# Performance work log

Measured on AMD Instinct MI355X. Metric: run time of the kernel, lower is better.

The kernel has to match this reference:

```python
import math
import jax, jax.numpy as jnp
import numpy as np

G_RATIO = 0.5
TB_FACTOR = 1e-3


def _expand(x):
    # x: [B,H,W]; 3x3 all-ones-except-center neighbor conv (same filter for every sample)
    k = jnp.ones((1, 1, 3, 3), x.dtype).at[0, 0, 1, 1].set(0.0)
    y = jax.lax.conv_general_dilated(x[:, None], k, (1, 1), 'SAME')
    return y[:, 0]


def _st_softmax_noexp(val):
    # straight-through normalized selection over flattened map
    B = val.shape[0]
    v = val.reshape(B, -1)
    y = v / v.sum(-1, keepdims=True)
    ind = jnp.argmax(y, -1)
    y_hard = jax.nn.one_hot(ind, y.shape[-1], dtype=y.dtype)
    y = y + jax.lax.stop_gradient(y_hard - y)
    return y.reshape(val.shape)


def _heuristic(gm):
    # gm: [B,H,W] one-hot goal maps -> Chebyshev + tb*Euclidean distance field
    B, H, W = gm.shape
    loc = jnp.stack(jnp.meshgrid(jnp.arange(H), jnp.arange(W), indexing='ij'), 0).astype(gm.dtype)  # [2,H,W]
    loc_e = loc.reshape(2, -1)[None]                      # [1,2,HW]
    goal_loc = jnp.einsum('kij,bij->bk', loc, gm)[:, :, None]  # [B,2,1]
    d = jnp.abs(loc_e - goal_loc)                         # [B,2,HW]
    h = d.sum(1) - d.min(1)
    euc = jnp.sqrt(((loc_e - goal_loc) ** 2).sum(1))
    return (h + TB_FACTOR * euc).reshape(B, H, W)


def _forward_core(cost_maps, start_maps, goal_maps, obstacles_maps):
    cm, sm, gm, om = cost_maps[:, 0], start_maps[:, 0], goal_maps[:, 0], obstacles_maps[:, 0]
    B, H, W = cm.shape
    h = _heuristic(gm) + cm
    goal_idx = jnp.argmax(gm.reshape(B, -1), -1)
    parents0 = jnp.broadcast_to(goal_idx[:, None].astype(cm.dtype), (B, H * W))
    inv_sqrt = 1.0 / math.sqrt(W)
    Tmax = W * W

    def step(carry, i):
        g, open_m, hist, parents, done, t = carry
        f = G_RATIO * g + (1.0 - G_RATIO) * h
        f_exp = jnp.exp(-f * inv_sqrt) * open_m
        snm = _st_softmax_noexp(f_exp)
        dist = (snm * gm).sum((1, 2), keepdims=True)
        unsolved = (dist < 1e-8).astype(cm.dtype)
        hist_n = jnp.clip(hist + snm, 0.0, 1.0)
        open_n = jnp.clip(open_m - unsolved * snm, 0.0, 1.0)
        nb = _expand(snm) * om
        g2 = _expand((g + cm) * snm)
        idx = ((1.0 - open_n) * (1.0 - hist_n) + open_n * (g > g2).astype(cm.dtype)) * nb
        idx = jax.lax.stop_gradient(idx)
        g_n = jax.lax.stop_gradient(g2 * idx + g * (1.0 - idx))
        open_n = jax.lax.stop_gradient(jnp.clip(open_n + idx, 0.0, 1.0))
        idx_f = idx.reshape(B, -1)
        new_par = jnp.argmax(snm.reshape(B, -1), -1)[:, None].astype(cm.dtype)
        par_n = new_par * idx_f + parents * (1.0 - idx_f)
        done_n = jnp.all(unsolved == 0)
        sel = lambda new, old: jnp.where(done, old, new)  # emulate the torch early break
        carry_n = (sel(g_n, g), sel(open_n, open_m), sel(hist_n, hist), sel(par_n, parents),
                   jnp.logical_or(done, done_n), jnp.where(done, t, i))
        return carry_n, None

    init = (jnp.zeros_like(sm), sm, jnp.zeros_like(sm), parents0,
            jnp.array(False), jnp.array(0, jnp.int32))
    (g, open_m, hist, parents, done, t), _ = jax.lax.scan(
        step, init, jnp.arange(Tmax, dtype=jnp.int32))
    return hist[:, None], parents, t


def _backtrack(goal_maps, parents, t):
    gm = goal_maps[:, 0]
    B, H, W = gm.shape
    par_i = parents.astype(jnp.int32)
    goal_f = gm.reshape(B, -1).astype(jnp.int32)
    loc = (par_i * goal_f).sum(-1)
    rng = jnp.arange(B)

    def bt(i, val):
        path, loc = val
        path = path.at[rng, loc].set(1)
        loc = jnp.take_along_axis(par_i, loc[:, None], -1)[:, 0]
        return (path, loc)

    path, _ = jax.lax.fori_loop(0, t, bt, (goal_f, loc))
    return path.reshape(B, 1, H, W)


def setup_inputs() -> dict:
    key = jax.random.key(0)
    k1, k2, k3, k4 = jax.random.split(key, 4)
    B, H, W = 16, 32, 32
    cost_maps = jax.random.uniform(k1, (B, 1, H, W), dtype=jnp.float32)
    sidx = jax.random.randint(k2, (B,), 0, H * W)
    gidx = jax.random.randint(k3, (B,), 0, H * W)
    gidx = jnp.where(gidx == sidx, (gidx + 1) % (H * W), gidx)
    start_maps = jax.nn.one_hot(sidx, H * W, dtype=jnp.float32).reshape(B, 1, H, W)
    goal_maps = jax.nn.one_hot(gidx, H * W, dtype=jnp.float32).reshape(B, 1, H, W)
    obstacles_maps = (jax.random.uniform(k4, (B, 1, H, W)) > 0.05).astype(jnp.float32)
    obstacles_maps = jnp.clip(obstacles_maps + start_maps + goal_maps, 0.0, 1.0)
    return {'cost_maps': cost_maps, 'start_maps': start_maps,
            'goal_maps': goal_maps, 'obstacles_maps': obstacles_maps}


def reference(cost_maps, start_maps, goal_maps, obstacles_maps):
    histories, parents, t = _forward_core(cost_maps, start_maps, goal_maps, obstacles_maps)
    path_maps = _backtrack(goal_maps, parents, t)
    return histories, path_maps
```

## Files before the change

kernel.cpp:

```cpp
#include <hip/hip_runtime.h>
#include <math.h>

#define HH 32
#define WW 32
#define HW 1024
#define NB 16
#define TMAXS 1024

typedef unsigned long long ull;

__device__ __forceinline__ float keyval(float g, float h) {
#pragma clang fp contract(off)
  const float INV = 0.17677669529663687f;
  float f = 0.5f * g + 0.5f * h;
  return expf(-f * INV);
}

template <int CTRL>
__device__ __forceinline__ double dpp_fmax64(double x) {
  ull u = (ull)__double_as_longlong(x);
  int lo = (int)(unsigned)u;
  int hi = (int)(unsigned)(u >> 32);
  int lo2 = __builtin_amdgcn_update_dpp(0, lo, CTRL, 0xF, 0xF, false);
  int hi2 = __builtin_amdgcn_update_dpp(0, hi, CTRL, 0xF, 0xF, false);
  double y = __longlong_as_double(
      (long long)(((ull)(unsigned)hi2 << 32) | (unsigned)lo2));
  return fmax(x, y);
}

extern "C" __global__ void __launch_bounds__(64) astar_fused(
    const float* __restrict__ cm_g, const float* __restrict__ sm_g,
    const float* __restrict__ gm_g, const float* __restrict__ om_g,
    float* __restrict__ out) {
#pragma clang fp contract(off)
  const int b = blockIdx.x;
  const int lane = threadIdx.x;

  __shared__ __align__(16) ull key2[HW];
  __shared__ __align__(16) float4 gch[HW];
  __shared__ unsigned int flg[HW];
  __shared__ unsigned int par[HW];

  const float* cm = cm_g + b * HW;
  const float* sm = sm_g + b * HW;
  const float* gm = gm_g + b * HW;
  const float* om = om_g + b * HW;

  float cml[16], oml[16];
  int gi = -1, si = -1;
#pragma unroll
  for (int q = 0; q < 16; ++q) {
    const int cell = q * 64 + lane;
    const float c = cm[cell], s = sm[cell], g = gm[cell], o = om[cell];
    cml[q] = c;
    oml[q] = o;
    if (g > 0.5f) gi = cell;
    if (s > 0.5f) si = cell;
  }
#pragma unroll
  for (int m = 32; m >= 1; m >>= 1) {
    const int og = __shfl_xor(gi, m, 64);
    const int os = __shfl_xor(si, m, 64);
    gi = (og > gi) ? og : gi;
    si = (os > si) ? os : si;
  }
  const int goal = gi, start = si;

  const float grf = (float)(goal >> 5), gcf = (float)(goal & 31);
#pragma unroll
  for (int q = 0; q < 16; ++q) {
    const int cell = q * 64 + lane;
    const float rr = (float)(cell >> 5), cc = (float)(cell & 31);
    const float dr = fabsf(rr - grf), dc = fabsf(cc - gcf);
    const float h0 = (dr + dc) - fminf(dr, dc);
    const float euc = sqrtf(dr * dr + dc * dc);
    const float t1 = 0.001f * euc;
    const float hh = h0 + t1;
    const float hf = hh + cml[q];
    gch[cell] = make_float4(0.0f, cml[q], cml[q], hf);
    unsigned f = (oml[q] > 0.5f) ? 1u : 0u;
    ull pk = (ull)(1023 - cell);
    if (cell == start) {
      f |= 2u;
      pk |= (ull)__double_as_longlong((double)keyval(0.0f, hf));
    }
    flg[cell] = f;
    par[cell] = (unsigned)goal;
    key2[cell] = pk;
  }

  int dro = 0, dco = 0;
  if (lane < 8) {
    const int k = (lane < 4) ? lane : lane + 1;
    dro = k / 3 - 1;
    dco = k % 3 - 1;
  }
  const float* gchf = (const float*)gch;
  __builtin_amdgcn_wave_barrier();

#pragma unroll 1
  for (int step = 0; step < TMAXS; ++step) {
    double s[8];
#pragma unroll
    for (int q = 0; q < 8; ++q) {
      const ulonglong2 v = *(const ulonglong2*)&key2[q * 128 + lane * 2];
      s[q] = fmax(__longlong_as_double((long long)v.x),
                  __longlong_as_double((long long)v.y));
    }
    const double t0 = fmax(s[0], s[1]), t1 = fmax(s[2], s[3]);
    const double t2 = fmax(s[4], s[5]), t3 = fmax(s[6], s[7]);
    double mm = fmax(fmax(t0, t1), fmax(t2, t3));

    mm = dpp_fmax64<0x111>(mm);
    mm = dpp_fmax64<0x112>(mm);
    mm = dpp_fmax64<0x114>(mm);
    mm = dpp_fmax64<0x118>(mm);
    mm = dpp_fmax64<0x142>(mm);
    mm = dpp_fmax64<0x143>(mm);
    const int lo63 =
        __builtin_amdgcn_readlane((int)(unsigned)(ull)__double_as_longlong(mm), 63);
    const int sel = 1023 - (lo63 & 1023);

    if (sel == goal) {
      if (lane == 0) flg[goal] |= 4u;
      break;
    }

    if (lane < 9) {
      if (lane < 8) {
        const int nr = (sel >> 5) + dro, nc = (sel & 31) + dco;
        if ((unsigned)nr < 32u && (unsigned)nc < 32u) {
          const int n = (nr << 5) | nc;
          const unsigned f = flg[n];
          const float4 v = gch[n];
          const float g2 = gchf[4 * sel + 2];
          const bool upd =
              (f & 1u) && (((f & 6u) == 0u) || (((f & 2u) != 0u) && (v.x > g2)));
          if (upd) {
            gch[n] = make_float4(g2, v.y, g2 + v.y, v.w);
            flg[n] = f | 2u;
            par[n] = (unsigned)sel;
            const float kk = keyval(g2, v.w);
            key2[n] = ((ull)__double_as_longlong((double)kk)) | (ull)(1023 - n);
          }
        }
      } else {
        const unsigned fs = flg[sel];
        flg[sel] = (fs | 4u) & ~2u;
        key2[sel] = (ull)(1023 - sel);
      }
    }
    __builtin_amdgcn_wave_barrier();
  }

  __builtin_amdgcn_wave_barrier();
  if (lane == 0) {
    const unsigned pv = par[goal];
    par[goal] = pv | 0x80000000u;
    unsigned loc = pv & 1023u;
#pragma unroll 1
    for (int i = 0; i < HW; ++i) {
      const unsigned v = par[loc];
      if (v & 0x80000000u) break;
      par[loc] = v | 0x80000000u;
      loc = v & 1023u;
    }
  }
  __builtin_amdgcn_wave_barrier();

#pragma unroll
  for (int q = 0; q < 4; ++q) {
    const int base = q * 256 + lane * 4;
    float4 hv, pv;
    hv.x = (flg[base + 0] & 4u) ? 1.0f : 0.0f;
    hv.y = (flg[base + 1] & 4u) ? 1.0f : 0.0f;
    hv.z = (flg[base + 2] & 4u) ? 1.0f : 0.0f;
    hv.w = (flg[base + 3] & 4u) ? 1.0f : 0.0f;
    pv.x = (par[base + 0] >> 31) ? 1.0f : 0.0f;
    pv.y = (par[base + 1] >> 31) ? 1.0f : 0.0f;
    pv.z = (par[base + 2] >> 31) ? 1.0f : 0.0f;
    pv.w = (par[base + 3] >> 31) ? 1.0f : 0.0f;
    *(float4*)(out + b * HW + base) = hv;
    *(float4*)(out + NB * HW + b * HW + base) = pv;
  }
}

extern "C" void kernel_launch(void* const* d_in, const int* in_sizes, int n_in,
                              void* d_out, int out_size, void* d_ws,
                              size_t ws_size, hipStream_t stream) {
  const float* cm = (const float*)d_in[0];
  const float* sm = (const float*)d_in[1];
  const float* gm = (const float*)d_in[2];
  const float* om = (const float*)d_in[3];
  float* out = (float*)d_out;
  hipLaunchKernelGGL(astar_fused, dim3(NB), dim3(64), 0, stream, cm, sm, gm,
                     om, out);
}
```

Before: 79.87 us.

## Keep open-set keys in registers and overlap neighbor expansion with max reduction

Each lane now keeps its slice of the packed open-set keys in registers. The per-step max reduction is computed from those registers, with the selected cell masked out and the neighbor updates folded in, so it overlaps with the neighbor LDS loads and no longer waits on a full LDS re-read. The key reload is moved after the update barrier, off the critical path of the next selection, and the first selected cell is taken directly from the start index. The input loads and shared-memory initialisation are also vectorised to float4/uint4, at the cost of more register pressure and more complex control flow.

```diff
diff --git a/kernel.cpp b/kernel.cpp
--- a/kernel.cpp
+++ b/kernel.cpp
@@ -1,13 +1,18 @@
 #include <hip/hip_runtime.h>
 #include <math.h>
 
-#define HH 32
-#define WW 32
 #define HW 1024
 #define NB 16
 #define TMAXS 1024
 
 typedef unsigned long long ull;
+
+__device__ __forceinline__ double u2d(ull u) {
+  return __longlong_as_double((long long)u);
+}
+__device__ __forceinline__ ull d2u(double d) {
+  return (ull)__double_as_longlong(d);
+}
 
 __device__ __forceinline__ float keyval(float g, float h) {
 #pragma clang fp contract(off)
@@ -18,13 +23,12 @@
 
 template <int CTRL>
 __device__ __forceinline__ double dpp_fmax64(double x) {
-  ull u = (ull)__double_as_longlong(x);
+  ull u = d2u(x);
   int lo = (int)(unsigned)u;
   int hi = (int)(unsigned)(u >> 32);
   int lo2 = __builtin_amdgcn_update_dpp(0, lo, CTRL, 0xF, 0xF, false);
   int hi2 = __builtin_amdgcn_update_dpp(0, hi, CTRL, 0xF, 0xF, false);
-  double y = __longlong_as_double(
-      (long long)(((ull)(unsigned)hi2 << 32) | (unsigned)lo2));
+  double y = u2d(((ull)(unsigned)hi2 << 32) | (unsigned)lo2);
   return fmax(x, y);
 }
 
@@ -38,24 +42,31 @@
 
   __shared__ __align__(16) ull key2[HW];
   __shared__ __align__(16) float4 gch[HW];
-  __shared__ unsigned int flg[HW];
-  __shared__ unsigned int par[HW];
+  __shared__ __align__(16) unsigned flg[HW];
+  __shared__ __align__(16) unsigned par[HW];
+  const float* gchf = (const float*)gch;
 
   const float* cm = cm_g + b * HW;
   const float* sm = sm_g + b * HW;
   const float* gm = gm_g + b * HW;
   const float* om = om_g + b * HW;
 
-  float cml[16], oml[16];
+  float4 c4[4], o4[4];
   int gi = -1, si = -1;
 #pragma unroll
-  for (int q = 0; q < 16; ++q) {
-    const int cell = q * 64 + lane;
-    const float c = cm[cell], s = sm[cell], g = gm[cell], o = om[cell];
-    cml[q] = c;
-    oml[q] = o;
-    if (g > 0.5f) gi = cell;
-    if (s > 0.5f) si = cell;
+  for (int q = 0; q < 4; ++q) {
+    const int base = q * 256 + lane * 4;
+    c4[q] = *(const float4*)(cm + base);
+    o4[q] = *(const float4*)(om + base);
+    const float4 s4 = *(const float4*)(sm + base);
+    const float4 g4 = *(const float4*)(gm + base);
+    const float sv[4] = {s4.x, s4.y, s4.z, s4.w};
+    const float gv[4] = {g4.x, g4.y, g4.z, g4.w};
+#pragma unroll
+    for (int j = 0; j < 4; ++j) {
+      if (gv[j] > 0.5f) gi = base + j;
+      if (sv[j] > 0.5f) si = base + j;
+    }
   }
 #pragma unroll
   for (int m = 32; m >= 1; m >>= 1) {
@@ -68,26 +79,45 @@
 
   const float grf = (float)(goal >> 5), gcf = (float)(goal & 31);
 #pragma unroll
-  for (int q = 0; q < 16; ++q) {
-    const int cell = q * 64 + lane;
-    const float rr = (float)(cell >> 5), cc = (float)(cell & 31);
-    const float dr = fabsf(rr - grf), dc = fabsf(cc - gcf);
-    const float h0 = (dr + dc) - fminf(dr, dc);
-    const float euc = sqrtf(dr * dr + dc * dc);
-    const float t1 = 0.001f * euc;
-    const float hh = h0 + t1;
-    const float hf = hh + cml[q];
-    gch[cell] = make_float4(0.0f, cml[q], cml[q], hf);
-    unsigned f = (oml[q] > 0.5f) ? 1u : 0u;
-    ull pk = (ull)(1023 - cell);
-    if (cell == start) {
-      f |= 2u;
-      pk |= (ull)__double_as_longlong((double)keyval(0.0f, hf));
-    }
-    flg[cell] = f;
-    par[cell] = (unsigned)goal;
-    key2[cell] = pk;
-  }
+  for (int q = 0; q < 4; ++q) {
+    const int base = q * 256 + lane * 4;
+    const float cv[4] = {c4[q].x, c4[q].y, c4[q].z, c4[q].w};
+    const float ov[4] = {o4[q].x, o4[q].y, o4[q].z, o4[q].w};
+    ull pk[4];
+    unsigned fv[4];
+#pragma unroll
+    for (int j = 0; j < 4; ++j) {
+      const int cell = base + j;
+      const float rr = (float)(cell >> 5), cc = (float)(cell & 31);
+      const float dr = fabsf(rr - grf), dc = fabsf(cc - gcf);
+      const float h0 = (dr + dc) - fminf(dr, dc);
+      const float euc = sqrtf(dr * dr + dc * dc);
+      const float t1 = 0.001f * euc;
+      const float hh = h0 + t1;
+      const float hf = hh + cv[j];
+      gch[cell] = make_float4(0.0f, cv[j], cv[j], hf);
+      fv[j] = (ov[j] > 0.5f) ? 1u : 0u;
+      pk[j] = (ull)(1023 - cell);
+      if (cell == start) {
+        fv[j] |= 2u;
+        pk[j] |= d2u((double)keyval(0.0f, hf));
+      }
+    }
+    *(uint4*)&flg[base] = make_uint4(fv[0], fv[1], fv[2], fv[3]);
+    *(uint4*)&par[base] =
+        make_uint4((unsigned)goal, (unsigned)goal, (unsigned)goal, (unsigned)goal);
+    ulonglong2 k01, k23;
+    k01.x = pk[0]; k01.y = pk[1];
+    k23.x = pk[2]; k23.y = pk[3];
+    *(ulonglong2*)&key2[base] = k01;
+    *(ulonglong2*)&key2[base + 2] = k23;
+  }
+  __builtin_amdgcn_wave_barrier();
+
+  ulonglong2 r[8];
+#pragma unroll
+  for (int q = 0; q < 8; ++q)
+    r[q] = *(const ulonglong2*)&key2[q * 128 + lane * 2];
 
   int dro = 0, dco = 0;
   if (lane < 8) {
@@ -95,75 +125,82 @@
     dro = k / 3 - 1;
     dco = k % 3 - 1;
   }
-  const float* gchf = (const float*)gch;
-  __builtin_amdgcn_wave_barrier();
+
+  int sel = start;
+  bool reached = false;
 
 #pragma unroll 1
   for (int step = 0; step < TMAXS; ++step) {
-    double s[8];
+    if (sel == goal) { reached = true; break; }
+
+    const float g2 = gchf[4 * sel + 2];
+    int n = -1;
+    unsigned f = 0;
+    float4 v = make_float4(0.f, 0.f, 0.f, 0.f);
+    if (lane < 8) {
+      const int nr = (sel >> 5) + dro, nc = (sel & 31) + dco;
+      if ((unsigned)nr < 32u && (unsigned)nc < 32u) {
+        n = (nr << 5) | nc;
+        f = flg[n];
+        v = gch[n];
+      }
+    }
+    unsigned fs = 0;
+    if (lane == 8) fs = flg[sel];
+
+    double m = 0.0;
 #pragma unroll
     for (int q = 0; q < 8; ++q) {
-      const ulonglong2 v = *(const ulonglong2*)&key2[q * 128 + lane * 2];
-      s[q] = fmax(__longlong_as_double((long long)v.x),
-                  __longlong_as_double((long long)v.y));
-    }
-    const double t0 = fmax(s[0], s[1]), t1 = fmax(s[2], s[3]);
-    const double t2 = fmax(s[4], s[5]), t3 = fmax(s[6], s[7]);
-    double mm = fmax(fmax(t0, t1), fmax(t2, t3));
-
-    mm = dpp_fmax64<0x111>(mm);
-    mm = dpp_fmax64<0x112>(mm);
-    mm = dpp_fmax64<0x114>(mm);
-    mm = dpp_fmax64<0x118>(mm);
-    mm = dpp_fmax64<0x142>(mm);
-    mm = dpp_fmax64<0x143>(mm);
-    const int lo63 =
-        __builtin_amdgcn_readlane((int)(unsigned)(ull)__double_as_longlong(mm), 63);
-    const int sel = 1023 - (lo63 & 1023);
-
-    if (sel == goal) {
-      if (lane == 0) flg[goal] |= 4u;
-      break;
-    }
-
-    if (lane < 9) {
-      if (lane < 8) {
-        const int nr = (sel >> 5) + dro, nc = (sel & 31) + dco;
-        if ((unsigned)nr < 32u && (unsigned)nc < 32u) {
-          const int n = (nr << 5) | nc;
-          const unsigned f = flg[n];
-          const float4 v = gch[n];
-          const float g2 = gchf[4 * sel + 2];
-          const bool upd =
-              (f & 1u) && (((f & 6u) == 0u) || (((f & 2u) != 0u) && (v.x > g2)));
-          if (upd) {
-            gch[n] = make_float4(g2, v.y, g2 + v.y, v.w);
-            flg[n] = f | 2u;
-            par[n] = (unsigned)sel;
-            const float kk = keyval(g2, v.w);
-            key2[n] = ((ull)__double_as_longlong((double)kk)) | (ull)(1023 - n);
-          }
-        }
-      } else {
-        const unsigned fs = flg[sel];
-        flg[sel] = (fs | 4u) & ~2u;
-        key2[sel] = (ull)(1023 - sel);
+      const int base = q * 128 + lane * 2;
+      const ull a = (base == sel) ? (ull)(1023 - base) : r[q].x;
+      const ull c = (base + 1 == sel) ? (ull)(1022 - base) : r[q].y;
+      m = fmax(m, fmax(u2d(a), u2d(c)));
+    }
+
+    if (lane < 8 && n >= 0) {
+      const bool upd =
+          (f & 1u) && (((f & 6u) == 0u) || (((f & 2u) != 0u) && (v.x > g2)));
+      if (upd) {
+        gch[n] = make_float4(g2, v.y, g2 + v.y, v.w);
+        flg[n] = f | 2u;
+        par[n] = (unsigned)sel;
+        const ull pk = d2u((double)keyval(g2, v.w)) | (ull)(1023 - n);
+        key2[n] = pk;
+        m = fmax(m, u2d(pk));
       }
     }
+    if (lane == 8) {
+      flg[sel] = (fs | 4u) & ~2u;
+      key2[sel] = (ull)(1023 - sel);
+    }
     __builtin_amdgcn_wave_barrier();
-  }
-
+
+#pragma unroll
+    for (int q = 0; q < 8; ++q)
+      r[q] = *(const ulonglong2*)&key2[q * 128 + lane * 2];
+
+    m = dpp_fmax64<0x111>(m);
+    m = dpp_fmax64<0x112>(m);
+    m = dpp_fmax64<0x114>(m);
+    m = dpp_fmax64<0x118>(m);
+    m = dpp_fmax64<0x142>(m);
+    m = dpp_fmax64<0x143>(m);
+    const int lo63 = __builtin_amdgcn_readlane((int)(unsigned)d2u(m), 63);
+    sel = 1023 - (lo63 & 1023);
+  }
+  if (reached && lane == 0) flg[goal] |= 4u;
   __builtin_amdgcn_wave_barrier();
+
   if (lane == 0) {
     const unsigned pv = par[goal];
     par[goal] = pv | 0x80000000u;
     unsigned loc = pv & 1023u;
 #pragma unroll 1
     for (int i = 0; i < HW; ++i) {
-      const unsigned v = par[loc];
-      if (v & 0x80000000u) break;
-      par[loc] = v | 0x80000000u;
-      loc = v & 1023u;
+      const unsigned w = par[loc];
+      if (w & 0x80000000u) break;
+      par[loc] = w | 0x80000000u;
+      loc = w & 1023u;
     }
   }
   __builtin_amdgcn_wave_barrier();
```

Measured after the change: 78.40 us. Within noise of the previous version (-1.8%).
